# Performance work log

Measured on AMD Instinct MI355X. Metric: run time of the kernel, lower is better.

## Reference

```python
import jax, jax.numpy as jnp
import numpy as np

B, S, NSAMP = 64, 21, 3000
HID, SEC, N, ATT = 500, 6, 2, 128
OUT, NPROTO, NCLS, NHEAD = 128, 25, 5, 4


def _pe(length, d):
    pos = np.arange(length, dtype=np.float32)[:, None]
    div = np.exp(np.arange(0, d, 2, dtype=np.float32) * (-np.log(10000.0) / d))
    pe = np.zeros((length, d), np.float32)
    pe[:, 0::2] = np.sin(pos * div)
    pe[:, 1::2] = np.cos(pos * div)
    return jnp.asarray(pe)


def _ln(x, g, b, eps=1e-5):
    m = x.mean(-1, keepdims=True)
    v = ((x - m) ** 2).mean(-1, keepdims=True)
    return (x - m) * jax.lax.rsqrt(v + eps) * g + b


def _conv1d(x, w, b):
    y = jax.lax.conv_general_dilated(x, w, (1,), [(1, 1)], dimension_numbers=('NCH', 'OIH', 'NCH'))
    return y + b[None, :, None]


def _maxpool(x, k):
    n, c, l = x.shape
    m = (l // k) * k  # torch MaxPool1d floors
    return x[:, :, :m].reshape(n, c, l // k, k).max(-1)


def _bn_eval(x, g, b, eps=1e-5):
    # eval-mode BatchNorm1d with running_mean=0, running_var=1
    return x * (g / np.sqrt(1.0 + eps))[None, :, None] + b[None, :, None]


def setup_inputs():
    key = jax.random.key(0)
    ks = jax.random.split(key, 16)
    def w(i, shape, s=0.02):
        return jax.random.normal(ks[i], shape, jnp.float32) * s
    u = jax.random.uniform(ks[0], (B * S * N, SEC), jnp.float32, 1e-6, 1.0 - 1e-6)
    return dict(
        x=jax.random.normal(ks[1], (B, S, 1, NSAMP), jnp.float32),
        gumbel=-jnp.log(-jnp.log(u)),
        wq=w(2, (HID, ATT * N)), wk=w(3, (HID, ATT * N)),
        w1=w(4, (32, 1, 3)), b1=jnp.zeros(32), bn1_g=jnp.ones(32), bn1_b=jnp.zeros(32),
        w2=w(5, (64, 32, 3)), b2=jnp.zeros(64), bn2_g=jnp.ones(64), bn2_b=jnp.zeros(64),
        w3=w(6, (128, 64, 3)), b3=jnp.zeros(128), bn3_g=jnp.ones(128), bn3_b=jnp.zeros(128),
        fc_w=w(7, (768, 256)), fc_b=jnp.zeros(256),
        fc2_w=w(8, (256, OUT)), fc2_b=jnp.zeros(OUT),
        protos=w(9, (NPROTO, OUT), 1.0),
        in_w=w(10, (OUT, 3 * OUT)), in_b=jnp.zeros(3 * OUT),
        out_w=w(11, (OUT, OUT)), out_b=jnp.zeros(OUT),
        ln1_g=jnp.ones(OUT), ln1_b=jnp.zeros(OUT),
        ln2_g=jnp.ones(OUT), ln2_b=jnp.zeros(OUT),
        ff1_w=w(12, (OUT, OUT)), ff1_b=jnp.zeros(OUT),
        ff2_w=w(13, (OUT, OUT)), ff2_b=jnp.zeros(OUT),
        clf_w=w(14, (OUT, NCLS)), clf_b=jnp.zeros(NCLS),
    )


def reference(x, gumbel, wq, wk, w1, b1, bn1_g, bn1_b, w2, b2, bn2_g, bn2_b,
              w3, b3, bn3_g, bn3_b, fc_w, fc_b, fc2_w, fc2_b, protos,
              in_w, in_b, out_w, out_b, ln1_g, ln1_b, ln2_g, ln2_b,
              ff1_w, ff1_b, ff2_w, ff2_b, clf_w, clf_b):
    bs = B * S
    # ---- HardAttentionLayer (gumbel hard sampling over SEC sections) ----
    xr = x.reshape(bs, SEC, HID)                       # (BS, 6, 500)
    xp = xr + _pe(100, HID)[None, :SEC]
    q = (xp @ wq).reshape(bs, SEC, N, ATT).transpose(0, 2, 1, 3)  # bnsh
    k = (xp @ wk).reshape(bs, SEC, N, ATT).transpose(0, 2, 1, 3)
    att = jnp.einsum('bnsh,bnth->bnst', q, k) / (HID ** 0.5)
    logits = (att.sum(-1) / SEC).reshape(bs * N, SEC)
    y_soft = jax.nn.softmax(logits + gumbel)           # tau = 1.0
    y_hard = jax.nn.one_hot(jnp.argmax(y_soft, -1), SEC, dtype=y_soft.dtype)
    alphas = (y_hard - jax.lax.stop_gradient(y_soft) + y_soft).reshape(bs, N, SEC)
    sampled = jnp.einsum('bns,bsh->bnh', alphas, xr)   # (BS, N, 500)
    # ---- conv/MLP epoch encoder (eval: dropout off, BN running stats) ----
    c = sampled.reshape(bs * N, 1, HID)
    c = _bn_eval(_maxpool(jax.nn.relu(_conv1d(c, w1, b1)), 4), bn1_g, bn1_b)
    c = _bn_eval(_maxpool(jax.nn.relu(_conv1d(c, w2, b2)), HID // 100), bn2_g, bn2_b)
    c = _bn_eval(_maxpool(jax.nn.relu(_conv1d(c, w3, b3)), 4), bn3_g, bn3_b)
    c = c.reshape(bs * N, -1) @ fc_w + fc_b
    z = c @ fc2_w + fc2_b                              # (B*S*N, 128)
    # ---- PrototypeLayer: VQ codebook lookup with straight-through ----
    d2 = (z * z).sum(1, keepdims=True) + (protos * protos).sum(1) - 2.0 * z @ protos.T
    proto = protos[jnp.argmin(d2, 1)]
    proto_st = z + jax.lax.stop_gradient(proto - z)
    # ---- SequenceEncoder: 1-layer post-norm transformer ----
    p_clf = proto_st.reshape(B, S, N, OUT).sum(2) / N  # (B, S, 128)
    h = p_clf + _pe(1024, OUT)[None, :S]
    qkv = h @ in_w + in_b
    qh, kh, vh = [t.reshape(B, S, NHEAD, OUT // NHEAD) for t in jnp.split(qkv, 3, -1)]
    sc = jnp.einsum('bqhd,bkhd->bhqk', qh, kh) / ((OUT // NHEAD) ** 0.5)
    ctx = jnp.einsum('bhqk,bkhd->bqhd', jax.nn.softmax(sc, -1), vh).reshape(B, S, OUT)
    h = _ln(h + ctx @ out_w + out_b, ln1_g, ln1_b)
    ff = jax.nn.relu(h @ ff1_w + ff1_b) @ ff2_w + ff2_b
    h = _ln(h + ff, ln2_g, ln2_b)
    return (h.reshape(-1, OUT) @ clf_w + clf_b).reshape(B, S, NCLS)
```

## Files before the change

kernel.cpp:

```cpp
#include <hip/hip_runtime.h>
#include <math.h>

#define BB 64
#define SS 21
#define NSAMP 3000
#define HID 500
#define SECN 6
#define NN 2
#define OUTD 128
#define NPROTO 25
#define NCLS 5
#define NHEAD 4
#define BS (BB*SS)
#define NSAMPLE (BS*NN)

#define C500 (-0.0184206807439523674f)
#define C128 (-0.07195578415606439f)
#define LSCALE 0.00745355992499929898f

#define WS_W2HI 5376
#define WS_W2LO 8448
#define WS_W3HI 11520
#define WS_W3LO 23808
#define WS_P3   36096
#define WS_C3   55296
#define WS_WQT  55424
#define WS_V    727424
#define WS_CTX  (WS_V + 520192)

typedef __attribute__((ext_vector_type(8))) short short8;
typedef __attribute__((ext_vector_type(4))) short short4v;
typedef __attribute__((ext_vector_type(4))) float floatx4;

__device__ __forceinline__ short f2bf(float f) {
  unsigned u = __float_as_uint(f);
  u += 0x7FFF + ((u >> 16) & 1);
  return (short)(u >> 16);
}
__device__ __forceinline__ float bf2f(short h) {
  return __uint_as_float(((unsigned)(unsigned short)h) << 16);
}

__global__ __launch_bounds__(256) void prep_all_kernel(
    const float* __restrict__ w2, const float* __restrict__ w3,
    short* __restrict__ w2hi, short* __restrict__ w2lo,
    short* __restrict__ w3hi, short* __restrict__ w3lo,
    const float* __restrict__ protos, const float* __restrict__ fc2w,
    const float* __restrict__ fcw, const float* __restrict__ fcb,
    const float* __restrict__ fc2b,
    float* __restrict__ P3, float* __restrict__ c3,
    const float* __restrict__ wq, float* __restrict__ wqT) {
  __shared__ __align__(16) float p2row[256];
  __shared__ float red[256];
  __shared__ float tile[64][65];
  const int t = threadIdx.x;
  if (blockIdx.x < 120) {
    int idx = blockIdx.x * 256 + t;
    if (idx < 6144) {
      int ic = idx & 31, ck = idx >> 5, k = ck % 3, c = ck / 3;
      float v = w2[c * 96 + ic * 3 + k];
      int dst = (((k * 4 + (c >> 4)) * 64) + ((ic >> 3) * 16 + (c & 15))) * 8 + (ic & 7);
      short hi = f2bf(v);
      short lo = f2bf(v - bf2f(hi));
      w2hi[dst] = hi; w2lo[dst] = lo;
    } else if (idx < 30720) {
      int j = idx - 6144;
      int ic = j & 63, ck = j >> 6, k = ck % 3, c = ck / 3;
      float v = w3[(c * 64 + ic) * 3 + k];
      int s = k * 2 + (ic >> 5);
      int dst = (((s * 8 + (c >> 4)) * 64) + (((ic & 31) >> 3) * 16 + (c & 15))) * 8 + (ic & 7);
      short hi = f2bf(v);
      short lo = f2bf(v - bf2f(hi));
      w3hi[dst] = hi; w3lo[dst] = lo;
    }
    return;
  }
  if (blockIdx.x >= 145) {
    int tid = blockIdx.x - 145;
    int h0 = (tid >> 2) * 64, c0 = (tid & 3) * 64;
    for (int e = t; e < 4096; e += 256) {
      int i = e >> 6, j = e & 63;
      if (h0 + i < 500) tile[j][i] = wq[(h0 + i) * 256 + c0 + j];
    }
    __syncthreads();
    for (int e = t; e < 4096; e += 256) {
      int c = e >> 6, hh = e & 63;
      if (h0 + hh < 500) wqT[(c0 + c) * 500 + h0 + hh] = tile[c][hh];
    }
    return;
  }
  const int p = blockIdx.x - 120, j = t;
  {
    const float4* pr = reinterpret_cast<const float4*>(protos + p * 128);
    const float4* wr = reinterpret_cast<const float4*>(fc2w + j * 128);
    float4 a4 = make_float4(0.f, 0.f, 0.f, 0.f);
    for (int c4 = 0; c4 < 32; c4++) {
      float4 a = pr[c4], b = wr[c4];
      a4.x += a.x * b.x; a4.y += a.y * b.y; a4.z += a.z * b.z; a4.w += a.w * b.w;
    }
    float v = (a4.x + a4.y) + (a4.z + a4.w);
    p2row[j] = v;
    float contrib = v * fcb[j];
    if (j < 128) {
      float pv = protos[p * 128 + j];
      contrib += pv * fc2b[j] - 0.5f * pv * pv;
    }
    red[j] = contrib;
  }
  __syncthreads();
  for (int s = 128; s > 0; s >>= 1) {
    if (j < s) red[j] += red[j + s];
    __syncthreads();
  }
  if (j == 0) c3[p] = red[0];
  for (int k = j; k < 768; k += 256) {
    const float4* fr = reinterpret_cast<const float4*>(fcw + k * 256);
    const float4* p2 = reinterpret_cast<const float4*>(p2row);
    float4 a4 = make_float4(0.f, 0.f, 0.f, 0.f);
    for (int j4 = 0; j4 < 64; j4++) {
      float4 a = p2[j4], b = fr[j4];
      a4.x += a.x * b.x; a4.y += a.y * b.y; a4.z += a.z * b.z; a4.w += a.w * b.w;
    }
    P3[p * 768 + k] = (a4.x + a4.y) + (a4.z + a4.w);
  }
}

#define MBX 4
__global__ __launch_bounds__(512) void attn_b_kernel(
    const float* __restrict__ x, const float* __restrict__ wk,
    const float* __restrict__ wqT, float* __restrict__ v) {
  __shared__ __align__(16) float pesum[500];
  __shared__ __align__(16) float xs[MBX * 500];
  __shared__ __align__(16) float ksp[2 * 256 * MBX];
  __shared__ __align__(16) float ks_t[256 * MBX];
  const int blk = blockIdx.x, t = threadIdx.x;

  if (t < 125) {
    float div0 = expf((float)(4 * t) * C500);
    float div1 = expf((float)(4 * t + 2) * C500);
    float s0 = 0.f, c0 = 0.f, s1 = 0.f, c1 = 0.f;
#pragma unroll
    for (int s = 0; s < SECN; s++) {
      float a0 = (float)s * div0, a1 = (float)s * div1;
      s0 += sinf(a0); c0 += cosf(a0);
      s1 += sinf(a1); c1 += cosf(a1);
    }
    reinterpret_cast<float4*>(pesum)[t] = make_float4(s0, c0, s1, c1);
  }
  __syncthreads();

  for (int e = t; e < MBX * 125; e += 512) {
    int m = e / 125, h4 = e % 125;
    const float4* xr = reinterpret_cast<const float4*>(x) + (blk * MBX + m) * 750;
    float4 a = xr[h4];
#pragma unroll
    for (int s = 1; s < SECN; s++) {
      float4 b = xr[s * 125 + h4];
      a.x += b.x; a.y += b.y; a.z += b.z; a.w += b.w;
    }
    float4 pe = reinterpret_cast<float4*>(pesum)[h4];
    a.x += pe.x; a.y += pe.y; a.z += pe.z; a.w += pe.w;
    reinterpret_cast<float4*>(xs)[m * 125 + h4] = a;
  }
  __syncthreads();

  {
    int c = t & 255, kh = t >> 8;
    float acc[MBX];
#pragma unroll
    for (int m = 0; m < MBX; m++) acc[m] = 0.f;
    int b4 = kh ? 63 : 0, e4 = kh ? 125 : 63;
    const float4* xsb = reinterpret_cast<const float4*>(xs);
    for (int i4 = b4; i4 < e4; i4++) {
      int i = i4 * 4;
      float w0 = wk[(i + 0) * 256 + c];
      float w1 = wk[(i + 1) * 256 + c];
      float w2v = wk[(i + 2) * 256 + c];
      float w3v = wk[(i + 3) * 256 + c];
#pragma unroll
      for (int m = 0; m < MBX; m++) {
        float4 xv = xsb[m * 125 + i4];
        acc[m] += xv.x * w0 + xv.y * w1 + xv.z * w2v + xv.w * w3v;
      }
    }
#pragma unroll
    for (int m = 0; m < MBX; m++)
      ksp[(kh * 256 + c) * MBX + m] = acc[m];
  }
  __syncthreads();
  for (int e = t; e < 256 * MBX; e += 512) ks_t[e] = ksp[e] + ksp[256 * MBX + e];
  __syncthreads();

  if (t < 500) {
    int h = t;
#pragma unroll
    for (int n = 0; n < 2; n++) {
      float acc[MBX];
#pragma unroll
      for (int m = 0; m < MBX; m++) acc[m] = 0.f;
      const float* wcol = wqT + (n * 128) * 500 + h;
      const floatx4* ktb = (const floatx4*)ks_t + n * 128;
      for (int c = 0; c < 128; c++) {
        float w = wcol[c * 500];
        floatx4 k0 = ktb[c];
        acc[0] += w * k0[0]; acc[1] += w * k0[1]; acc[2] += w * k0[2]; acc[3] += w * k0[3];
      }
#pragma unroll
      for (int m = 0; m < MBX; m++)
        v[((blk * MBX + m) * 2 + n) * 500 + h] = acc[m];
    }
  }
}

__global__ __launch_bounds__(192) void attn_c_kernel(
    const float* __restrict__ x, const float* __restrict__ v,
    const float* __restrict__ gumbel, int* __restrict__ sec_idx) {
  __shared__ float lgsh[NN][SECN];
  const int bs = blockIdx.x, t = threadIdx.x;
  const int s = t >> 5, lane = t & 31;
  const float4* x4 = reinterpret_cast<const float4*>(x) + bs * 750 + s * 125;
  const float4* v0 = reinterpret_cast<const float4*>(v) + bs * 250;
  const float4* v1 = v0 + 125;
  float a0 = 0.f, a1 = 0.f;
  for (int h4 = lane; h4 < 125; h4 += 32) {
    float4 xv = x4[h4];
    float div0 = expf((float)(4 * h4) * C500);
    float div1 = expf((float)(4 * h4 + 2) * C500);
    float ang0 = (float)s * div0, ang1 = (float)s * div1;
    xv.x += sinf(ang0); xv.y += cosf(ang0);
    xv.z += sinf(ang1); xv.w += cosf(ang1);
    float4 w0 = v0[h4], w1 = v1[h4];
    a0 += xv.x * w0.x + xv.y * w0.y + xv.z * w0.z + xv.w * w0.w;
    a1 += xv.x * w1.x + xv.y * w1.y + xv.z * w1.z + xv.w * w1.w;
  }
#pragma unroll
  for (int m = 16; m >= 1; m >>= 1) {
    a0 += __shfl_xor(a0, m);
    a1 += __shfl_xor(a1, m);
  }
  if (lane == 0) {
    lgsh[0][s] = a0 * LSCALE + gumbel[(bs * 2 + 0) * SECN + s];
    lgsh[1][s] = a1 * LSCALE + gumbel[(bs * 2 + 1) * SECN + s];
  }
  __syncthreads();
  if (t < 2) {
    int best = 0; float bv = lgsh[t][0];
    for (int i = 1; i < SECN; i++) {
      float q = lgsh[t][i];
      if (q > bv) { bv = q; best = i; }
    }
    sec_idx[bs * 2 + t] = best;
  }
}

#define CONV_LDS 53568
#define ST2P 68
__global__ __launch_bounds__(512, 3) void conv_kernel(
    const float* __restrict__ x, const int* __restrict__ sec_idx,
    const float* __restrict__ w1, const float* __restrict__ b1,
    const float* __restrict__ bn1g, const float* __restrict__ bn1b,
    const short* __restrict__ w2hi, const short* __restrict__ w2lo,
    const float* __restrict__ b2,
    const float* __restrict__ bn2g, const float* __restrict__ bn2b,
    const short* __restrict__ w3hi, const short* __restrict__ w3lo,
    const float* __restrict__ b3,
    const float* __restrict__ bn3g, const float* __restrict__ bn3b,
    const float* __restrict__ P3, const float* __restrict__ c3,
    int* __restrict__ proto_idx) {
  __shared__ __align__(16) char smem[CONV_LDS];
  short* act1_hi  = (short*)smem;
  short* act1_lo  = (short*)(smem + 10400);
  short* act2p_hi = (short*)smem;
  short* act2p_lo = (short*)(smem + 4624);
  float* featsh   = (float*)(smem + 9792);
  float* sc25     = (float*)(smem + 12864);
  float* in0p  = (float*)(smem + 20800);
  float* act2t = (float*)(smem + 20800);
  float* act3t = (float*)(smem + 20800);

  const int sample = blockIdx.x;
  const int t = threadIdx.x;
  const int bsIdx = sample >> 1;
  const float bnscale = rsqrtf(1.0f + 1e-5f);
  const int wv = t >> 6, l = t & 63, lr = l & 15, lg2 = l >> 4;

  {
    int sec = sec_idx[sample];
    const float* src = &x[bsIdx * NSAMP + sec * HID];
    if (t < 512) in0p[t] = (t >= 1 && t <= 500) ? src[t - 1] : 0.f;
    if (t < 200) {
      int r = t / 40; r = (r == 0) ? 0 : 125 + r;
      int idx = r * 40 + t % 40;
      act1_hi[idx] = 0; act1_lo[idx] = 0;
    }
  }
  __syncthreads();

  {
    int ic = t & 31;
    float w0 = w1[ic * 3], w1v = w1[ic * 3 + 1], w2v = w1[ic * 3 + 2];
    float bb = b1[ic];
    float g = bn1g[ic] * bnscale, be = bn1b[ic];
    for (int p = t >> 5; p < 125; p += 16) {
      int base = 4 * p;
      float xm1 = in0p[base], x0 = in0p[base + 1], x1 = in0p[base + 2],
            x2 = in0p[base + 3], x3 = in0p[base + 4], x4 = in0p[base + 5];
      float a0 = bb + w0 * xm1 + w1v * x0 + w2v * x1;
      float a1 = bb + w0 * x0  + w1v * x1 + w2v * x2;
      float a2 = bb + w0 * x1  + w1v * x2 + w2v * x3;
      float a3 = bb + w0 * x2  + w1v * x3 + w2v * x4;
      float m = fmaxf(fmaxf(fmaxf(fmaxf(a0, a1), a2), a3), 0.f);
      float v = m * g + be;
      short hi = f2bf(v);
      short lo = f2bf(v - bf2f(hi));
      act1_hi[(p + 1) * 40 + ic] = hi;
      act1_lo[(p + 1) * 40 + ic] = lo;
    }
  }
  __syncthreads();

  {
    floatx4 acc[4];
#pragma unroll
    for (int m = 0; m < 4; m++) acc[m] = (floatx4){0.f, 0.f, 0.f, 0.f};
#pragma unroll
    for (int s = 0; s < 3; s++) {
      short8 Ah[4], Al[4], Bh, Bl;
#pragma unroll
      for (int m = 0; m < 4; m++) {
        int aoff = ((s * 4 + m) * 64 + l) * 8;
        Ah[m] = *(const short8*)(w2hi + aoff);
        Al[m] = *(const short8*)(w2lo + aoff);
      }
      {
        int boff = (wv * 16 + lr + s) * 40 + lg2 * 8;
        Bh = *(const short8*)(act1_hi + boff);
        Bl = *(const short8*)(act1_lo + boff);
      }
#pragma unroll
      for (int m = 0; m < 4; m++) {
        acc[m] = __builtin_amdgcn_mfma_f32_16x16x32_bf16(Ah[m], Bh, acc[m], 0, 0, 0);
        acc[m] = __builtin_amdgcn_mfma_f32_16x16x32_bf16(Ah[m], Bl, acc[m], 0, 0, 0);
        acc[m] = __builtin_amdgcn_mfma_f32_16x16x32_bf16(Al[m], Bh, acc[m], 0, 0, 0);
      }
    }
#pragma unroll
    for (int m = 0; m < 4; m++) {
      int p = wv * 16 + lr;
      int swz = (m * 4 + lg2) ^ lr;
      *(floatx4*)(act2t + p * 64 + swz * 4) = acc[m];
    }
  }
  __syncthreads();

  {
    if (t < 153) {
      for (int i = t; i < 612; i += 153) {
        int r = i / ST2P; r = (r == 0) ? 0 : 25 + r;
        int idx = r * ST2P + i % ST2P;
        act2p_hi[idx] = 0; act2p_lo[idx] = 0;
      }
    }
    int ic = t & 63;
    float bb = b2[ic], g = bn2g[ic] * bnscale, be = bn2b[ic];
#define A2T(r, c) act2t[(r) * 64 + ((((c) >> 2) ^ ((r) & 15)) << 2) + ((c) & 3)]
    for (int pw = t >> 6; pw < 25; pw += 8) {
      int base = 5 * pw;
      float m = A2T(base, ic);
      m = fmaxf(m, A2T(base + 1, ic));
      m = fmaxf(m, A2T(base + 2, ic));
      m = fmaxf(m, A2T(base + 3, ic));
      m = fmaxf(m, A2T(base + 4, ic));
      float v = fmaxf(m + bb, 0.f) * g + be;
      short hi = f2bf(v);
      short lo = f2bf(v - bf2f(hi));
      act2p_hi[(pw + 1) * ST2P + ic] = hi;
      act2p_lo[(pw + 1) * ST2P + ic] = lo;
    }
#undef A2T
  }
  __syncthreads();

  {
    floatx4 acc[2];
#pragma unroll
    for (int nn = 0; nn < 2; nn++) acc[nn] = (floatx4){0.f, 0.f, 0.f, 0.f};
#pragma unroll
    for (int s = 0; s < 6; s++) {
      short8 Ah, Al, Bh[2], Bl[2];
      {
        int aoff = ((s * 8 + wv) * 64 + l) * 8;
        Ah = *(const short8*)(w3hi + aoff);
        Al = *(const short8*)(w3lo + aoff);
      }
#pragma unroll
      for (int nn = 0; nn < 2; nn++) {
        int boff = (nn * 16 + lr + (s >> 1)) * ST2P + (s & 1) * 32 + lg2 * 8;
        short4v h0 = *(const short4v*)(act2p_hi + boff);
        short4v h1 = *(const short4v*)(act2p_hi + boff + 4);
        short4v l0 = *(const short4v*)(act2p_lo + boff);
        short4v l1 = *(const short4v*)(act2p_lo + boff + 4);
        Bh[nn] = (short8){h0[0], h0[1], h0[2], h0[3], h1[0], h1[1], h1[2], h1[3]};
        Bl[nn] = (short8){l0[0], l0[1], l0[2], l0[3], l1[0], l1[1], l1[2], l1[3]};
      }
#pragma unroll
      for (int nn = 0; nn < 2; nn++) {
        acc[nn] = __builtin_amdgcn_mfma_f32_16x16x32_bf16(Ah, Bh[nn], acc[nn], 0, 0, 0);
        acc[nn] = __builtin_amdgcn_mfma_f32_16x16x32_bf16(Ah, Bl[nn], acc[nn], 0, 0, 0);
        acc[nn] = __builtin_amdgcn_mfma_f32_16x16x32_bf16(Al, Bh[nn], acc[nn], 0, 0, 0);
      }
    }
#pragma unroll
    for (int nn = 0; nn < 2; nn++) {
      int p = nn * 16 + lr;
      *(floatx4*)(act3t + p * 132 + wv * 16 + lg2 * 4) = acc[nn];
    }
  }
  __syncthreads();

  {
    int c = t & 127;
    float bb = b3[c], g = bn3g[c] * bnscale, be = bn3b[c];
    for (int pw = t >> 7; pw < 6; pw += 4) {
      int base = 4 * pw;
      float m = act3t[base * 132 + c];
      m = fmaxf(m, act3t[(base + 1) * 132 + c]);
      m = fmaxf(m, act3t[(base + 2) * 132 + c]);
      m = fmaxf(m, act3t[(base + 3) * 132 + c]);
      float v = fmaxf(m + bb, 0.f) * g + be;
      featsh[c * 6 + pw] = v;
    }
  }
  __syncthreads();

  if (t < NPROTO * 8) {
    int p = t >> 3, part = t & 7;
    const float4* pr = reinterpret_cast<const float4*>(P3 + p * 768 + part * 96);
    const float4* fr = reinterpret_cast<const float4*>(featsh + part * 96);
    float4 a4 = make_float4(0.f, 0.f, 0.f, 0.f);
#pragma unroll
    for (int i = 0; i < 24; i++) {
      float4 w = pr[i], f = fr[i];
      a4.x += w.x * f.x; a4.y += w.y * f.y; a4.z += w.z * f.z; a4.w += w.w * f.w;
    }
    float a = (a4.x + a4.y) + (a4.z + a4.w);
    a += __shfl_xor(a, 1);
    a += __shfl_xor(a, 2);
    a += __shfl_xor(a, 4);
    if (part == 0) sc25[p] = a + c3[p];
  }
  __syncthreads();
  if (t == 0) {
    int best = 0; float bv = sc25[0];
    for (int i = 1; i < NPROTO; i++) {
      float v = sc25[i];
      if (v > bv) { bv = v; best = i; }
    }
    proto_idx[sample] = best;
  }
}

__global__ __launch_bounds__(256) void seq_qk_attn_kernel(
    const int* __restrict__ proto_idx, const float* __restrict__ protos,
    const float* __restrict__ inw, const float* __restrict__ inb,
    float* __restrict__ ctxbuf) {
  __shared__ __align__(16) float hsh[SS * OUTD];
  __shared__ float qs_[SS][32], ks_[SS][32], vs_[SS][32];
  __shared__ float sc_[SS][SS + 1];
  const int b = blockIdx.x >> 2, hd = blockIdx.x & 3;
  const int t = threadIdx.x;

  for (int o = t; o < SS * OUTD; o += 256) {
    int s = o >> 7, d = o & 127;
    int i0 = proto_idx[(b * SS + s) * 2];
    int i1 = proto_idx[(b * SS + s) * 2 + 1];
    float pc = 0.5f * (protos[i0 * OUTD + d] + protos[i1 * OUTD + d]);
    float div = expf((float)(2 * (d >> 1)) * C128);
    float ang = (float)s * div;
    float pe = (d & 1) ? cosf(ang) : sinf(ang);
    hsh[o] = pc + pe;
  }
  __syncthreads();

  for (int o = t; o < SS * 96; o += 256) {
    int s = o / 96, j = o % 96;
    int sec = j >> 5, dd = j & 31;
    int col = sec * 128 + hd * 32 + dd;
    float a = inb[col];
    const float4* hr = reinterpret_cast<const float4*>(&hsh[s * OUTD]);
    for (int d4 = 0; d4 < 32; d4++) {
      float4 h4 = hr[d4];
      int d = d4 * 4;
      a += h4.x * inw[(d + 0) * 384 + col] + h4.y * inw[(d + 1) * 384 + col]
         + h4.z * inw[(d + 2) * 384 + col] + h4.w * inw[(d + 3) * 384 + col];
    }
    if (sec == 0) qs_[s][dd] = a;
    else if (sec == 1) ks_[s][dd] = a;
    else vs_[s][dd] = a;
  }
  __syncthreads();

  for (int e = t; e < SS * SS; e += 256) {
    int qs = e / SS, ks = e % SS;
    float a = 0.f;
#pragma unroll
    for (int d = 0; d < 32; d++) a += qs_[qs][d] * ks_[ks][d];
    sc_[qs][ks] = a * 0.17677669529663689f;
  }
  __syncthreads();
  if (t < SS) {
    float mx = sc_[t][0];
    for (int i = 1; i < SS; i++) mx = fmaxf(mx, sc_[t][i]);
    float sum = 0.f;
    for (int i = 0; i < SS; i++) { float e = expf(sc_[t][i] - mx); sc_[t][i] = e; sum += e; }
    float inv = 1.f / sum;
    for (int i = 0; i < SS; i++) sc_[t][i] *= inv;
  }
  __syncthreads();
  for (int e = t; e < SS * 32; e += 256) {
    int qs = e >> 5, dd = e & 31;
    float a = 0.f;
#pragma unroll
    for (int ks = 0; ks < SS; ks++) a += sc_[qs][ks] * vs_[ks][dd];
    ctxbuf[(b * SS + qs) * OUTD + hd * 32 + dd] = a;
  }
}

__global__ __launch_bounds__(128) void seq_tail_kernel(
    const int* __restrict__ proto_idx, const float* __restrict__ protos,
    const float* __restrict__ ctxbuf,
    const float* __restrict__ outw, const float* __restrict__ outb,
    const float* __restrict__ ln1g, const float* __restrict__ ln1b,
    const float* __restrict__ ff1w, const float* __restrict__ ff1b,
    const float* __restrict__ ff2w, const float* __restrict__ ff2b,
    const float* __restrict__ ln2g, const float* __restrict__ ln2b,
    const float* __restrict__ clfw, const float* __restrict__ clfb,
    float* __restrict__ out) {
  __shared__ __align__(16) float rowA[OUTD];
  __shared__ __align__(16) float rowB[OUTD];
  __shared__ float lds2[2];
  const int bs = blockIdx.x, t = threadIdx.x;
  const int s = bs % SS;

  rowA[t] = ctxbuf[bs * OUTD + t];
  __syncthreads();
  float a = outb[t];
  {
    const float4* cr = reinterpret_cast<const float4*>(rowA);
    for (int e4 = 0; e4 < 32; e4++) {
      float4 c4 = cr[e4];
      int e = e4 * 4;
      a += c4.x * outw[(e + 0) * OUTD + t] + c4.y * outw[(e + 1) * OUTD + t]
         + c4.z * outw[(e + 2) * OUTD + t] + c4.w * outw[(e + 3) * OUTD + t];
    }
  }
  float hv;
  {
    int i0 = proto_idx[bs * 2], i1 = proto_idx[bs * 2 + 1];
    float pc = 0.5f * (protos[i0 * OUTD + t] + protos[i1 * OUTD + t]);
    float div = expf((float)(2 * (t >> 1)) * C128);
    float ang = (float)s * div;
    float pe = (t & 1) ? cosf(ang) : sinf(ang);
    hv = pc + pe;
  }
  float tmp = hv + a;
  {
    float v = tmp;
#pragma unroll
    for (int k = 32; k >= 1; k >>= 1) v += __shfl_xor(v, k);
    if ((t & 63) == 0) lds2[t >> 6] = v;
    __syncthreads();
    float m = (lds2[0] + lds2[1]) * (1.0f / OUTD);
    __syncthreads();
    float u = tmp - m;
    float w = u * u;
#pragma unroll
    for (int k = 32; k >= 1; k >>= 1) w += __shfl_xor(w, k);
    if ((t & 63) == 0) lds2[t >> 6] = w;
    __syncthreads();
    float var = (lds2[0] + lds2[1]) * (1.0f / OUTD);
    __syncthreads();
    rowA[t] = u * rsqrtf(var + 1e-5f) * ln1g[t] + ln1b[t];
  }
  __syncthreads();
  {
    float r = ff1b[t];
    const float4* hr = reinterpret_cast<const float4*>(rowA);
    for (int e4 = 0; e4 < 32; e4++) {
      float4 h4 = hr[e4];
      int e = e4 * 4;
      r += h4.x * ff1w[(e + 0) * OUTD + t] + h4.y * ff1w[(e + 1) * OUTD + t]
         + h4.z * ff1w[(e + 2) * OUTD + t] + h4.w * ff1w[(e + 3) * OUTD + t];
    }
    rowB[t] = fmaxf(r, 0.f);
  }
  __syncthreads();
  float tmp2;
  {
    float r = ff2b[t];
    const float4* cr = reinterpret_cast<const float4*>(rowB);
    for (int e4 = 0; e4 < 32; e4++) {
      float4 c4 = cr[e4];
      int e = e4 * 4;
      r += c4.x * ff2w[(e + 0) * OUTD + t] + c4.y * ff2w[(e + 1) * OUTD + t]
         + c4.z * ff2w[(e + 2) * OUTD + t] + c4.w * ff2w[(e + 3) * OUTD + t];
    }
    tmp2 = rowA[t] + r;
  }
  __syncthreads();
  {
    float v = tmp2;
#pragma unroll
    for (int k = 32; k >= 1; k >>= 1) v += __shfl_xor(v, k);
    if ((t & 63) == 0) lds2[t >> 6] = v;
    __syncthreads();
    float m = (lds2[0] + lds2[1]) * (1.0f / OUTD);
    __syncthreads();
    float u = tmp2 - m;
    float w = u * u;
#pragma unroll
    for (int k = 32; k >= 1; k >>= 1) w += __shfl_xor(w, k);
    if ((t & 63) == 0) lds2[t >> 6] = w;
    __syncthreads();
    float var = (lds2[0] + lds2[1]) * (1.0f / OUTD);
    rowA[t] = u * rsqrtf(var + 1e-5f) * ln2g[t] + ln2b[t];
  }
  __syncthreads();
  if (t < NCLS) {
    float acc = clfb[t];
    for (int d = 0; d < OUTD; d++) acc += rowA[d] * clfw[d * NCLS + t];
    out[bs * NCLS + t] = acc;
  }
}

extern "C" void kernel_launch(void* const* d_in, const int* in_sizes, int n_in,
                              void* d_out, int out_size, void* d_ws, size_t ws_size,
                              hipStream_t stream) {
  const float* x     = (const float*)d_in[0];
  const float* gum   = (const float*)d_in[1];
  const float* wq    = (const float*)d_in[2];
  const float* wk    = (const float*)d_in[3];
  const float* w1    = (const float*)d_in[4];
  const float* b1    = (const float*)d_in[5];
  const float* bn1g  = (const float*)d_in[6];
  const float* bn1b  = (const float*)d_in[7];
  const float* w2    = (const float*)d_in[8];
  const float* b2    = (const float*)d_in[9];
  const float* bn2g  = (const float*)d_in[10];
  const float* bn2b  = (const float*)d_in[11];
  const float* w3    = (const float*)d_in[12];
  const float* b3    = (const float*)d_in[13];
  const float* bn3g  = (const float*)d_in[14];
  const float* bn3b  = (const float*)d_in[15];
  const float* fcw   = (const float*)d_in[16];
  const float* fcb   = (const float*)d_in[17];
  const float* fc2w  = (const float*)d_in[18];
  const float* fc2b  = (const float*)d_in[19];
  const float* prot  = (const float*)d_in[20];
  const float* inw   = (const float*)d_in[21];
  const float* inb   = (const float*)d_in[22];
  const float* outw  = (const float*)d_in[23];
  const float* outb  = (const float*)d_in[24];
  const float* ln1g  = (const float*)d_in[25];
  const float* ln1b  = (const float*)d_in[26];
  const float* ln2g  = (const float*)d_in[27];
  const float* ln2b  = (const float*)d_in[28];
  const float* ff1w  = (const float*)d_in[29];
  const float* ff1b  = (const float*)d_in[30];
  const float* ff2w  = (const float*)d_in[31];
  const float* ff2b  = (const float*)d_in[32];
  const float* clfw  = (const float*)d_in[33];
  const float* clfb  = (const float*)d_in[34];
  float* out = (float*)d_out;

  int* sec_idx   = (int*)d_ws;
  int* proto_idx = sec_idx + NSAMPLE;
  short* w2hi = (short*)((float*)d_ws + WS_W2HI);
  short* w2lo = (short*)((float*)d_ws + WS_W2LO);
  short* w3hi = (short*)((float*)d_ws + WS_W3HI);
  short* w3lo = (short*)((float*)d_ws + WS_W3LO);
  float* P3   = (float*)d_ws + WS_P3;
  float* c3   = (float*)d_ws + WS_C3;
  float* wqT  = (float*)d_ws + WS_WQT;
  float* vbuf = (float*)d_ws + WS_V;
  float* ctxb = (float*)d_ws + WS_CTX;

  hipLaunchKernelGGL(prep_all_kernel, dim3(177), dim3(256), 0, stream,
                     w2, w3, w2hi, w2lo, w3hi, w3lo,
                     prot, fc2w, fcw, fcb, fc2b, P3, c3, wq, wqT);
  hipLaunchKernelGGL(attn_b_kernel, dim3(BS / MBX), dim3(512), 0, stream,
                     x, wk, wqT, vbuf);
  hipLaunchKernelGGL(attn_c_kernel, dim3(BS), dim3(192), 0, stream,
                     x, vbuf, gum, sec_idx);
  hipLaunchKernelGGL(conv_kernel, dim3(NSAMPLE), dim3(512), 0, stream,
                     x, sec_idx, w1, b1, bn1g, bn1b, w2hi, w2lo, b2, bn2g, bn2b,
                     w3hi, w3lo, b3, bn3g, bn3b, P3, c3, proto_idx);
  hipLaunchKernelGGL(seq_qk_attn_kernel, dim3(BB * NHEAD), dim3(256), 0, stream,
                     proto_idx, prot, inw, inb, ctxb);
  hipLaunchKernelGGL(seq_tail_kernel, dim3(BS), dim3(128), 0, stream,
                     proto_idx, prot, ctxb, outw, outb, ln1g, ln1b,
                     ff1w, ff1b, ff2w, ff2b, ln2g, ln2b, clfw, clfb, out);
}
```

Baseline: 185.3 us.

## Split conv2 MFMA stage into two halves to shrink LDS and raise occupancy

```diff
diff --git a/kernel.cpp b/kernel.cpp
--- a/kernel.cpp
+++ b/kernel.cpp
@@ -253,9 +253,9 @@
   }
 }
 
-#define CONV_LDS 53568
+#define CONV_LDS 46944
 #define ST2P 68
-__global__ __launch_bounds__(512, 3) void conv_kernel(
+__global__ __launch_bounds__(512, 6) void conv_kernel(
     const float* __restrict__ x, const int* __restrict__ sec_idx,
     const float* __restrict__ w1, const float* __restrict__ b1,
     const float* __restrict__ bn1g, const float* __restrict__ bn1b,
@@ -270,13 +270,14 @@
   __shared__ __align__(16) char smem[CONV_LDS];
   short* act1_hi  = (short*)smem;
   short* act1_lo  = (short*)(smem + 10400);
-  short* act2p_hi = (short*)smem;
-  short* act2p_lo = (short*)(smem + 4624);
-  float* featsh   = (float*)(smem + 9792);
-  float* sc25     = (float*)(smem + 12864);
-  float* in0p  = (float*)(smem + 20800);
-  float* act2t = (float*)(smem + 20800);
-  float* act3t = (float*)(smem + 20800);
+  short* act2p_hi = (short*)(smem + 20800);
+  short* act2p_lo = (short*)(smem + 25424);
+  float* featsh   = (float*)smem;
+  float* sc25     = (float*)(smem + 3072);
+  float* in0p  = (float*)(smem + 30048);
+  float* act2t = (float*)(smem + 30048);
+  float* act3t = (float*)(smem + 30048);
+  float* bnd   = (float*)(smem + 46432);
 
   const int sample = blockIdx.x;
   const int t = threadIdx.x;
@@ -292,6 +293,14 @@
       int r = t / 40; r = (r == 0) ? 0 : 125 + r;
       int idx = r * 40 + t % 40;
       act1_hi[idx] = 0; act1_lo[idx] = 0;
+    }
+    if (t >= 256 && t < 256 + 153) {
+      int tt = t - 256;
+      for (int i = tt; i < 612; i += 153) {
+        int r = i / ST2P; r = (r == 0) ? 0 : 25 + r;
+        int idx = r * ST2P + i % ST2P;
+        act2p_hi[idx] = 0; act2p_lo[idx] = 0;
+      }
     }
   }
   __syncthreads();
@@ -319,67 +328,94 @@
   }
   __syncthreads();
 
-  {
-    floatx4 acc[4];
-#pragma unroll
-    for (int m = 0; m < 4; m++) acc[m] = (floatx4){0.f, 0.f, 0.f, 0.f};
-#pragma unroll
-    for (int s = 0; s < 3; s++) {
-      short8 Ah[4], Al[4], Bh, Bl;
-#pragma unroll
-      for (int m = 0; m < 4; m++) {
-        int aoff = ((s * 4 + m) * 64 + l) * 8;
-        Ah[m] = *(const short8*)(w2hi + aoff);
-        Al[m] = *(const short8*)(w2lo + aoff);
-      }
-      {
-        int boff = (wv * 16 + lr + s) * 40 + lg2 * 8;
-        Bh = *(const short8*)(act1_hi + boff);
-        Bl = *(const short8*)(act1_lo + boff);
-      }
-#pragma unroll
-      for (int m = 0; m < 4; m++) {
-        acc[m] = __builtin_amdgcn_mfma_f32_16x16x32_bf16(Ah[m], Bh, acc[m], 0, 0, 0);
-        acc[m] = __builtin_amdgcn_mfma_f32_16x16x32_bf16(Ah[m], Bl, acc[m], 0, 0, 0);
-        acc[m] = __builtin_amdgcn_mfma_f32_16x16x32_bf16(Al[m], Bh, acc[m], 0, 0, 0);
-      }
-    }
-#pragma unroll
-    for (int m = 0; m < 4; m++) {
-      int p = wv * 16 + lr;
-      int swz = (m * 4 + lg2) ^ lr;
-      *(floatx4*)(act2t + p * 64 + swz * 4) = acc[m];
-    }
-  }
-  __syncthreads();
-
-  {
-    if (t < 153) {
-      for (int i = t; i < 612; i += 153) {
-        int r = i / ST2P; r = (r == 0) ? 0 : 25 + r;
-        int idx = r * ST2P + i % ST2P;
-        act2p_hi[idx] = 0; act2p_lo[idx] = 0;
-      }
-    }
-    int ic = t & 63;
-    float bb = b2[ic], g = bn2g[ic] * bnscale, be = bn2b[ic];
 #define A2T(r, c) act2t[(r) * 64 + ((((c) >> 2) ^ ((r) & 15)) << 2) + ((c) & 3)]
-    for (int pw = t >> 6; pw < 25; pw += 8) {
-      int base = 5 * pw;
-      float m = A2T(base, ic);
-      m = fmaxf(m, A2T(base + 1, ic));
-      m = fmaxf(m, A2T(base + 2, ic));
-      m = fmaxf(m, A2T(base + 3, ic));
-      m = fmaxf(m, A2T(base + 4, ic));
-      float v = fmaxf(m + bb, 0.f) * g + be;
-      short hi = f2bf(v);
-      short lo = f2bf(v - bf2f(hi));
-      act2p_hi[(pw + 1) * ST2P + ic] = hi;
-      act2p_lo[(pw + 1) * ST2P + ic] = lo;
-    }
+#pragma unroll
+  for (int h = 0; h < 2; h++) {
+    {
+      int tl = wv & 3, mh = wv >> 2;
+      int lrow = tl * 16 + lr;
+      floatx4 acc[2];
+      acc[0] = (floatx4){0.f, 0.f, 0.f, 0.f};
+      acc[1] = acc[0];
+#pragma unroll
+      for (int s = 0; s < 3; s++) {
+        short8 Ah[2], Al[2], Bh, Bl;
+#pragma unroll
+        for (int j = 0; j < 2; j++) {
+          int m = mh * 2 + j;
+          int aoff = ((s * 4 + m) * 64 + l) * 8;
+          Ah[j] = *(const short8*)(w2hi + aoff);
+          Al[j] = *(const short8*)(w2lo + aoff);
+        }
+        {
+          int boff = (h * 64 + lrow + s) * 40 + lg2 * 8;
+          Bh = *(const short8*)(act1_hi + boff);
+          Bl = *(const short8*)(act1_lo + boff);
+        }
+#pragma unroll
+        for (int j = 0; j < 2; j++) {
+          acc[j] = __builtin_amdgcn_mfma_f32_16x16x32_bf16(Ah[j], Bh, acc[j], 0, 0, 0);
+          acc[j] = __builtin_amdgcn_mfma_f32_16x16x32_bf16(Ah[j], Bl, acc[j], 0, 0, 0);
+          acc[j] = __builtin_amdgcn_mfma_f32_16x16x32_bf16(Al[j], Bh, acc[j], 0, 0, 0);
+        }
+      }
+#pragma unroll
+      for (int j = 0; j < 2; j++) {
+        int m = mh * 2 + j;
+        int swz = (m * 4 + lg2) ^ lr;
+        *(floatx4*)(act2t + lrow * 64 + swz * 4) = acc[j];
+      }
+    }
+    __syncthreads();
+    {
+      int ic = t & 63;
+      float bb = b2[ic], g = bn2g[ic] * bnscale, be = bn2b[ic];
+      if (h == 0) {
+        for (int pw = t >> 6; pw < 13; pw += 8) {
+          if (pw < 12) {
+            int base = 5 * pw;
+            float m = A2T(base, ic);
+            m = fmaxf(m, A2T(base + 1, ic));
+            m = fmaxf(m, A2T(base + 2, ic));
+            m = fmaxf(m, A2T(base + 3, ic));
+            m = fmaxf(m, A2T(base + 4, ic));
+            float v = fmaxf(m + bb, 0.f) * g + be;
+            short hi = f2bf(v);
+            short lo = f2bf(v - bf2f(hi));
+            act2p_hi[(pw + 1) * ST2P + ic] = hi;
+            act2p_lo[(pw + 1) * ST2P + ic] = lo;
+          } else {
+            float m = A2T(60, ic);
+            m = fmaxf(m, A2T(61, ic));
+            m = fmaxf(m, A2T(62, ic));
+            m = fmaxf(m, A2T(63, ic));
+            bnd[ic] = m;
+          }
+        }
+      } else {
+        for (int pw = 12 + (t >> 6); pw < 25; pw += 8) {
+          float m;
+          if (pw == 12) {
+            m = fmaxf(bnd[ic], A2T(0, ic));
+          } else {
+            int base = 5 * pw - 64;
+            m = A2T(base, ic);
+            m = fmaxf(m, A2T(base + 1, ic));
+            m = fmaxf(m, A2T(base + 2, ic));
+            m = fmaxf(m, A2T(base + 3, ic));
+            m = fmaxf(m, A2T(base + 4, ic));
+          }
+          float v = fmaxf(m + bb, 0.f) * g + be;
+          short hi = f2bf(v);
+          short lo = f2bf(v - bf2f(hi));
+          act2p_hi[(pw + 1) * ST2P + ic] = hi;
+          act2p_lo[(pw + 1) * ST2P + ic] = lo;
+        }
+      }
+    }
+    __syncthreads();
+  }
 #undef A2T
-  }
-  __syncthreads();
 
   {
     floatx4 acc[2];
```

New measurement: 183.4 us. Within noise of the previous version (-1.0%).
